# Kernel optimization log

Hardware: AMD Instinct MI355X
Metric: run time of the kernel (lower is better)

## Reference

```python
import jax, jax.numpy as jnp
import numpy as np

NEAR_ZERO = 1e-6


def hat(w):
    # [..., 3] -> [..., 3, 3] skew-symmetric
    x, y, z = w[..., 0], w[..., 1], w[..., 2]
    O = jnp.zeros_like(x)
    return jnp.stack([jnp.stack([O, -z, y], -1),
                      jnp.stack([z, O, -x], -1),
                      jnp.stack([-y, x, O], -1)], -2)


def matrix_exp6(V):
    # V: [..., 6] twist (w, v) -> [..., 4, 4] SE(3) exp, with near-zero branch as in the torch code
    w, v = V[..., :3], V[..., 3:]
    theta = jnp.linalg.norm(w, axis=-1, keepdims=True)  # [..., 1]
    near = theta < NEAR_ZERO
    safe = jnp.where(near, 1.0, theta)
    Wh = hat(w / safe)
    Wh2 = Wh @ Wh
    t = theta[..., None]  # [..., 1, 1]
    I3 = jnp.eye(3, dtype=V.dtype)
    R = I3 + jnp.sin(t) * Wh + (1.0 - jnp.cos(t)) * Wh2
    R = jnp.where(near[..., None], I3, R)
    G = t * I3 + (1.0 - jnp.cos(t)) * Wh + (t - jnp.sin(t)) * Wh2
    p = jnp.einsum('...ij,...j->...i', G, v / safe)
    p = jnp.where(near, v, p)
    top = jnp.concatenate([R, p[..., None]], -1)
    bot = jnp.broadcast_to(jnp.array([0.0, 0.0, 0.0, 1.0], V.dtype), top.shape[:-2] + (1, 4))
    return jnp.concatenate([top, bot], -2)


def trans_inv(T):
    R = T[..., :3, :3]
    p = T[..., :3, 3]
    Rt = jnp.swapaxes(R, -1, -2)
    pinv = -jnp.einsum('...ij,...j->...i', Rt, p)
    top = jnp.concatenate([Rt, pinv[..., None]], -1)
    bot = jnp.broadcast_to(jnp.array([0.0, 0.0, 0.0, 1.0], T.dtype), top.shape[:-2] + (1, 4))
    return jnp.concatenate([top, bot], -2)


def adjoint(T):
    R = T[..., :3, :3]
    p = T[..., :3, 3]
    Z = jnp.zeros_like(R)
    top = jnp.concatenate([R, Z], -1)
    bot = jnp.concatenate([hat(p) @ R, R], -1)
    return jnp.concatenate([top, bot], -2)


def ad(V):
    W = hat(V[..., :3])
    Vh = hat(V[..., 3:])
    Z = jnp.zeros_like(W)
    top = jnp.concatenate([W, Z], -1)
    bot = jnp.concatenate([Vh, W], -1)
    return jnp.concatenate([top, bot], -2)


def inverse_dynamics(q, dq, ddq, g, Ftip, Alist, Mlist, Glist):
    # q, dq, ddq: [B, JN]; g: [3]; Ftip: [B, 6]; Alist: [JN, 6]; Mlist: [JN+1, 4, 4]; Glist: [JN, 6, 6]
    B, JN = q.shape
    Minv = trans_inv(Mlist)  # [JN+1, 4, 4]
    v0 = jnp.zeros((B, 6), q.dtype)
    a0 = jnp.concatenate([jnp.zeros((B, 3), q.dtype), jnp.broadcast_to(-g, (B, 3))], -1)

    # forward recursion over joints (sequential -> lax.scan), vectorized over batch
    def fwd_step(carry, xs):
        v, a = carry
        A_i, Minv_i, q_i, dq_i, ddq_i = xs
        T = matrix_exp6(-A_i[None, :] * q_i[:, None]) @ Minv_i  # [B, 4, 4]
        Ad = adjoint(T)
        v_new = jnp.einsum('bij,bj->bi', Ad, v) + A_i * dq_i[:, None]
        a_new = (jnp.einsum('bij,bj->bi', Ad, a)
                 + jnp.einsum('bij,j->bi', ad(v_new), A_i) * dq_i[:, None]
                 + A_i * ddq_i[:, None])
        return (v_new, a_new), (T, v_new, a_new)

    _, (Ts, vs, as_) = jax.lax.scan(fwd_step, (v0, a0), (Alist, Minv[:-1], q.T, dq.T, ddq.T))
    T_last = jnp.broadcast_to(Minv[-1], (B, 4, 4))
    AdNext = adjoint(jnp.concatenate([Ts[1:], T_last[None]], 0))  # [JN, B, 6, 6]

    # backward force recursion
    def bwd_step(F, xs):
        AdN, G_i, A_i, v_i, a_i = xs
        F_new = (jnp.einsum('bji,bj->bi', AdN, F)
                 + jnp.einsum('ij,bj->bi', G_i, a_i)
                 - jnp.einsum('bji,jk,bk->bi', ad(v_i), G_i, v_i))
        return F_new, F_new @ A_i

    _, tau = jax.lax.scan(bwd_step, Ftip, (AdNext, Glist, Alist, vs, as_), reverse=True)
    return tau.T  # [B, JN]


def setup_inputs() -> dict:
    key = jax.random.key(0)
    k = jax.random.split(key, 8)
    B, JN = 131072, 9
    q = jax.random.normal(k[0], (B, JN), jnp.float32)
    dq = jax.random.normal(k[1], (B, JN), jnp.float32)
    ddq = jax.random.normal(k[2], (B, JN), jnp.float32)
    Ftip = jax.random.normal(k[3], (B, 6), jnp.float32)
    g = jnp.array([0.0, 0.0, -9.8], jnp.float32)
    # screw axes with unit rotational part (revolute joints)
    w = jax.random.normal(k[4], (JN, 3), jnp.float32)
    w = w / jnp.linalg.norm(w, axis=-1, keepdims=True)
    vlin = jax.random.normal(k[5], (JN, 3), jnp.float32)
    Alist = jnp.concatenate([w, vlin], -1)
    # valid SE(3) home transforms
    Mlist = matrix_exp6(0.5 * jax.random.normal(k[6], (JN + 1, 6), jnp.float32))
    # SPD spatial inertias
    S = 0.3 * jax.random.normal(k[7], (JN, 6, 6), jnp.float32)
    Glist = S @ jnp.swapaxes(S, -1, -2) + jnp.eye(6, dtype=jnp.float32)
    return {"q": q, "dq": dq, "ddq": ddq, "g": g, "Ftip": Ftip,
            "Alist": Alist, "Mlist": Mlist, "Glist": Glist}


def reference(q, dq, ddq, g, Ftip, Alist, Mlist, Glist):
    return inverse_dynamics(q, dq, ddq, g, Ftip, Alist, Mlist, Glist)
```

## Files before the change

### kernel.cpp

```cpp
#include <hip/hip_runtime.h>
#include <math.h>

#define JN 9
#define BLK 128
#define BLK_FB 128
#define CPJ 84
#define CST_FLOATS (JN * CPJ + 12)

__device__ __forceinline__ void mat3_vec(const float* R, const float* x, float* y) {
    y[0] = R[0]*x[0] + R[1]*x[1] + R[2]*x[2];
    y[1] = R[3]*x[0] + R[4]*x[1] + R[5]*x[2];
    y[2] = R[6]*x[0] + R[7]*x[1] + R[8]*x[2];
}
__device__ __forceinline__ void mat3T_vec(const float* R, const float* x, float* y) {
    y[0] = R[0]*x[0] + R[3]*x[1] + R[6]*x[2];
    y[1] = R[1]*x[0] + R[4]*x[1] + R[7]*x[2];
    y[2] = R[2]*x[0] + R[5]*x[1] + R[8]*x[2];
}
__device__ __forceinline__ void cross3(const float* a, const float* b, float* o) {
    o[0] = a[1]*b[2] - a[2]*b[1];
    o[1] = a[2]*b[0] - a[0]*b[2];
    o[2] = a[0]*b[1] - a[1]*b[0];
}
__device__ __forceinline__ void adj_apply(const float* R, const float* p,
                                          const float* x, float* y) {
    float t[3], cr[3], rv[3];
    mat3_vec(R, x, t);
    cross3(p, t, cr);
    mat3_vec(R, x + 3, rv);
    y[0] = t[0]; y[1] = t[1]; y[2] = t[2];
    y[3] = cr[0] + rv[0]; y[4] = cr[1] + rv[1]; y[5] = cr[2] + rv[2];
}
__device__ __forceinline__ void adjT_apply(const float* R, const float* p,
                                           const float* x, float* y) {
    float cr[3], t[3];
    cross3(p, x + 3, cr);
    t[0] = x[0] - cr[0]; t[1] = x[1] - cr[1]; t[2] = x[2] - cr[2];
    mat3T_vec(R, t, y);
    mat3T_vec(R, x + 3, y + 3);
}

__global__ void prep_kernel(const float* __restrict__ A, const float* __restrict__ M,
                            const float* __restrict__ G, float* __restrict__ cst) {
    const int j = threadIdx.x;
    if (j < JN) {
        const float* Aj = A + j * 6;
        const float* Mj = M + j * 16;
        const float ax = Aj[0], ay = Aj[1], az = Aj[2];
        const float vx = Aj[3], vy = Aj[4], vz = Aj[5];
        float M1[9];
        for (int t = 0; t < 3; ++t)
            for (int c = 0; c < 3; ++c) M1[t*3+c] = Mj[c*4+t];
        const float K[9] = {0.f,-az,ay, az,0.f,-ax, -ay,ax,0.f};
        float M2[9];
        for (int r = 0; r < 3; ++r)
            for (int c = 0; c < 3; ++c)
                M2[r*3+c] = K[r*3+0]*M1[0*3+c] + K[r*3+1]*M1[1*3+c] + K[r*3+2]*M1[2*3+c];
        float t3[3];
        for (int c = 0; c < 3; ++c) t3[c] = ax*M1[0*3+c] + ay*M1[1*3+c] + az*M1[2*3+c];
        float M3[9];
        const float Aw[3] = {ax, ay, az};
        for (int r = 0; r < 3; ++r)
            for (int c = 0; c < 3; ++c) M3[r*3+c] = Aw[r] * t3[c];
        float Q1[9], Q3[9];
        for (int e = 0; e < 9; ++e) { Q1[e] = M1[e] - M3[e]; Q3[e] = M3[e]; }
        const float Mp[3] = {Mj[3], Mj[7], Mj[11]};
        const float d = ax*vx + ay*vy + az*vz;
        const float C[3] = {ay*vz - az*vy, az*vx - ax*vz, ax*vy - ay*vx};
        float q2m[3], q1m[3], q3m[3];
        mat3_vec(M2, Mp, q2m);
        mat3_vec(Q1, Mp, q1m);
        mat3_vec(Q3, Mp, q3m);
        float* o = cst + j * CPJ;
        for (int e = 0; e < 9; ++e) { o[e] = Q1[e]; o[9+e] = M2[e]; o[18+e] = Q3[e]; }
        o[27] = (vx - d*ax) - q2m[0]; o[28] = (vy - d*ay) - q2m[1]; o[29] = (vz - d*az) - q2m[2];
        o[30] = -C[0] - q1m[0];       o[31] = -C[1] - q1m[1];       o[32] = -C[2] - q1m[2];
        o[33] = d*ax;                 o[34] = d*ay;                 o[35] = d*az;
        o[36] = C[0] - q3m[0];        o[37] = C[1] - q3m[1];        o[38] = C[2] - q3m[2];
        for (int k = 0; k < 6; ++k)  o[39 + k] = Aj[k];
        const float* Gj = G + j * 36;
        for (int k = 0; k < 36; ++k) o[45 + k] = Gj[k];
    } else if (j == JN) {
        const float* M9 = M + JN * 16;
        float* o = cst + JN * CPJ;
        for (int r = 0; r < 3; ++r)
            for (int c = 0; c < 3; ++c) o[r*3+c] = M9[c*4+r];
        o[9] = M9[3]; o[10] = M9[7]; o[11] = M9[11];
    }
}

__device__ __forceinline__ void joint_step(const float* __restrict__ Cj,
                                           float qj, float dqj, float ddqj,
                                           float* XR, float* Xp, float* bv,
                                           float* ba, float* U,
                                           float* Bv, float* sig_out)
{
    const float phi = -qj;
    float s, c;
    __sincosf(phi, &s, &c);

    float TR[9], Tp[3];
#pragma unroll
    for (int e = 0; e < 9; ++e) TR[e] = c * Cj[e] + s * Cj[9 + e] + Cj[18 + e];
#pragma unroll
    for (int k = 0; k < 3; ++k)
        Tp[k] = s * Cj[27 + k] + c * Cj[30 + k] + phi * Cj[33 + k] + Cj[36 + k];

    {
        float nR[9], np[3];
#pragma unroll
        for (int r = 0; r < 3; ++r)
#pragma unroll
            for (int cc = 0; cc < 3; ++cc)
                nR[r*3+cc] = TR[r*3+0]*XR[0*3+cc] + TR[r*3+1]*XR[1*3+cc] + TR[r*3+2]*XR[2*3+cc];
        mat3_vec(TR, Xp, np);
#pragma unroll
        for (int e = 0; e < 9; ++e) XR[e] = nR[e];
        Xp[0] = np[0] + Tp[0]; Xp[1] = np[1] + Tp[1]; Xp[2] = np[2] + Tp[2];
    }

    const float Aw[3] = {Cj[39], Cj[40], Cj[41]};
    const float Av[3] = {Cj[42], Cj[43], Cj[44]};
    {
        float ip[3], tw[3], tv[3], cr[3];
        mat3T_vec(XR, Xp, ip);
        ip[0] = -ip[0]; ip[1] = -ip[1]; ip[2] = -ip[2];
        mat3T_vec(XR, Aw, tw);
        mat3T_vec(XR, Av, tv);
        cross3(ip, tw, cr);
        Bv[0] = tw[0]; Bv[1] = tw[1]; Bv[2] = tw[2];
        Bv[3] = cr[0] + tv[0]; Bv[4] = cr[1] + tv[1]; Bv[5] = cr[2] + tv[2];
    }

    *sig_out = Bv[0]*U[0] + Bv[1]*U[1] + Bv[2]*U[2]
             + Bv[3]*U[3] + Bv[4]*U[4] + Bv[5]*U[5];

#pragma unroll
    for (int k = 0; k < 6; ++k) bv[k] += Bv[k] * dqj;
    {
        float t0[3], t1[3], t2[3];
        cross3(bv, Bv, t0);
        cross3(bv + 3, Bv, t1);
        cross3(bv, Bv + 3, t2);
        ba[0] += t0[0]*dqj + Bv[0]*ddqj;
        ba[1] += t0[1]*dqj + Bv[1]*ddqj;
        ba[2] += t0[2]*dqj + Bv[2]*ddqj;
        ba[3] += (t1[0]+t2[0])*dqj + Bv[3]*ddqj;
        ba[4] += (t1[1]+t2[1])*dqj + Bv[4]*ddqj;
        ba[5] += (t1[2]+t2[2])*dqj + Bv[5]*ddqj;
    }

    float vl[6], al[6];
    adj_apply(XR, Xp, bv, vl);
    adj_apply(XR, Xp, ba, al);
    float Gv[6], Ga[6];
#pragma unroll
    for (int r = 0; r < 6; ++r) {
        float sv = 0.f, sa = 0.f;
#pragma unroll
        for (int kk = 0; kk < 6; ++kk) {
            const float gmv = Cj[45 + r*6 + kk];
            sv += gmv * vl[kk];
            sa += gmv * al[kk];
        }
        Gv[r] = sv; Ga[r] = sa;
    }
    float W[6];
    {
        float cw[3], cv[3], cb[3];
        cross3(vl, Gv, cw);
        cross3(vl + 3, Gv + 3, cv);
        cross3(vl, Gv + 3, cb);
        W[0] = Ga[0]+cw[0]+cv[0]; W[1] = Ga[1]+cw[1]+cv[1]; W[2] = Ga[2]+cw[2]+cv[2];
        W[3] = Ga[3]+cb[0];       W[4] = Ga[4]+cb[1];       W[5] = Ga[5]+cb[2];
    }
    {
        float S[6];
        adjT_apply(XR, Xp, W, S);
#pragma unroll
        for (int k = 0; k < 6; ++k) U[k] += S[k];
    }
}

__device__ __forceinline__ void tail_E(const float* __restrict__ W9,
                                       const float* XR, const float* Xp,
                                       const float* Ft, const float* U, float* E)
{
    float R9[9], p9[3];
#pragma unroll
    for (int r = 0; r < 3; ++r)
#pragma unroll
        for (int cc = 0; cc < 3; ++cc)
            R9[r*3+cc] = W9[r*3+0]*XR[0*3+cc] + W9[r*3+1]*XR[1*3+cc] + W9[r*3+2]*XR[2*3+cc];
    const float t[3] = {Xp[0] - W9[9], Xp[1] - W9[10], Xp[2] - W9[11]};
    mat3_vec(W9, t, p9);
    float Z[6];
    adjT_apply(R9, p9, Ft, Z);
#pragma unroll
    for (int k = 0; k < 6; ++k) E[k] = U[k] + Z[k];
}

__global__ void __launch_bounds__(BLK)
id_main(const float* __restrict__ q, const float* __restrict__ dq,
        const float* __restrict__ ddq, const float* __restrict__ gvec,
        const float* __restrict__ Ftip, const float* __restrict__ cst,
        float* __restrict__ out, int B)
{
    __shared__ float sQ[JN][BLK + 1];
    __shared__ float sB[JN * 6][BLK];
    __shared__ float sSig[JN][BLK];

    const int tid = threadIdx.x;
    const int b = blockIdx.x * BLK + tid;
    const float g0 = gvec[0], g1 = gvec[1], g2 = gvec[2];

#pragma unroll
    for (int j = 0; j < JN; ++j) sQ[j][tid] = q[(size_t)b * JN + j];

    float XR[9] = {1.f,0.f,0.f, 0.f,1.f,0.f, 0.f,0.f,1.f};
    float Xp[3] = {0.f, 0.f, 0.f};
    float bv[6] = {0.f,0.f,0.f,0.f,0.f,0.f};
    float ba[6] = {0.f, 0.f, 0.f, -g0, -g1, -g2};
    float U[6]  = {0.f,0.f,0.f,0.f,0.f,0.f};

#pragma unroll 1
    for (int j = 0; j < JN; ++j) {
        const float dqj  = dq[(size_t)b * JN + j];
        const float ddqj = ddq[(size_t)b * JN + j];
        const float qj   = sQ[j][tid];
        const float* Cj = cst + j * CPJ;
        float Bv[6], sg;
        joint_step(Cj, qj, dqj, ddqj, XR, Xp, bv, ba, U, Bv, &sg);
#pragma unroll
        for (int k = 0; k < 6; ++k) sB[j*6 + k][tid] = Bv[k];
        sSig[j][tid] = sg;
    }

    const float* W9 = cst + JN * CPJ;
    float Ft[6];
    __builtin_memcpy(Ft, Ftip + (size_t)b * 6, 6 * sizeof(float));
    float E[6];
    tail_E(W9, XR, Xp, Ft, U, E);

#pragma unroll
    for (int i = 0; i < JN; ++i) {
        float d = -sSig[i][tid];
#pragma unroll
        for (int k = 0; k < 6; ++k) d += sB[i*6 + k][tid] * E[k];
        sQ[i][tid] = d;
    }
    __syncthreads();
    const size_t base = (size_t)blockIdx.x * BLK * JN;
#pragma unroll
    for (int k = 0; k < JN; ++k) {
        const int g = tid + k * BLK;
        out[base + g] = sQ[g % JN][g / JN];
    }
}

__global__ void __launch_bounds__(BLK_FB)
id_kernel_fb(const float* __restrict__ q, const float* __restrict__ dq,
             const float* __restrict__ ddq, const float* __restrict__ gvec,
             const float* __restrict__ Ftip, const float* __restrict__ Alist,
             const float* __restrict__ Mlist, const float* __restrict__ Glist,
             float* __restrict__ out, int B)
{
    __shared__ float sB[JN * 6][BLK_FB];
    __shared__ float sSig[JN][BLK_FB];
    const int tid = threadIdx.x;
    const int b = blockIdx.x * BLK_FB + tid;
    if (b >= B) return;
    float XR[9] = {1.f,0.f,0.f, 0.f,1.f,0.f, 0.f,0.f,1.f};
    float Xp[3] = {0.f, 0.f, 0.f};
    float bv[6] = {0.f,0.f,0.f,0.f,0.f,0.f};
    float ba[6] = {0.f, 0.f, 0.f, -gvec[0], -gvec[1], -gvec[2]};
    float U[6]  = {0.f,0.f,0.f,0.f,0.f,0.f};
#pragma unroll 1
    for (int j = 0; j < JN; ++j) {
        const float* Am = Alist + j * 6;
        const float* Gm = Glist + j * 36;
        const float* Mj = Mlist + j * 16;
        float Aj[6];
#pragma unroll
        for (int k = 0; k < 6; ++k) Aj[k] = Am[k];
        const float qj = q[b*JN+j], dqj = dq[b*JN+j], ddqj = ddq[b*JN+j];
        const float w0 = -Aj[0]*qj, w1 = -Aj[1]*qj, w2 = -Aj[2]*qj;
        const float l0 = -Aj[3]*qj, l1 = -Aj[4]*qj, l2 = -Aj[5]*qj;
        const float th = sqrtf(w0*w0 + w1*w1 + w2*w2);
        const bool near = th < 1e-6f;
        const float safe = near ? 1.f : th;
        const float inv = __builtin_amdgcn_rcpf(safe);
        const float x = w0*inv, y = w1*inv, z = w2*inv;
        const float st = __sinf(th), ct = __cosf(th);
        const float s2 = 1.f - ct;
        const float a00 = -(z*z+y*y), a11 = -(z*z+x*x), a22 = -(y*y+x*x);
        const float a01 = x*y, a02 = x*z, a12 = y*z;
        float R[9];
        R[0]=1.f+s2*a00;   R[1]=-st*z+s2*a01; R[2]= st*y+s2*a02;
        R[3]= st*z+s2*a01; R[4]=1.f+s2*a11;   R[5]=-st*x+s2*a12;
        R[6]=-st*y+s2*a02; R[7]= st*x+s2*a12; R[8]=1.f+s2*a22;
        if (near) { R[0]=1;R[1]=0;R[2]=0;R[3]=0;R[4]=1;R[5]=0;R[6]=0;R[7]=0;R[8]=1; }
        const float g3 = th - st;
        const float u0 = l0*inv, u1 = l1*inv, u2 = l2*inv;
        float p0 = th*u0 + s2*(-z*u1+y*u2) + g3*(a00*u0+a01*u1+a02*u2);
        float p1 = th*u1 + s2*( z*u0-x*u2) + g3*(a01*u0+a11*u1+a12*u2);
        float p2 = th*u2 + s2*(-y*u0+x*u1) + g3*(a02*u0+a12*u1+a22*u2);
        if (near) { p0=l0; p1=l1; p2=l2; }
        float TR[9], Tp[3];
#pragma unroll
        for (int r = 0; r < 3; ++r)
#pragma unroll
            for (int cc = 0; cc < 3; ++cc)
                TR[r*3+cc] = R[r*3+0]*Mj[cc*4+0] + R[r*3+1]*Mj[cc*4+1] + R[r*3+2]*Mj[cc*4+2];
        const float mp0 = Mj[3], mp1 = Mj[7], mp2 = Mj[11];
        Tp[0] = p0 - (TR[0]*mp0 + TR[1]*mp1 + TR[2]*mp2);
        Tp[1] = p1 - (TR[3]*mp0 + TR[4]*mp1 + TR[5]*mp2);
        Tp[2] = p2 - (TR[6]*mp0 + TR[7]*mp1 + TR[8]*mp2);
        {
            float nR[9], np[3];
#pragma unroll
            for (int r = 0; r < 3; ++r)
#pragma unroll
                for (int cc = 0; cc < 3; ++cc)
                    nR[r*3+cc] = TR[r*3+0]*XR[0*3+cc] + TR[r*3+1]*XR[1*3+cc] + TR[r*3+2]*XR[2*3+cc];
            mat3_vec(TR, Xp, np);
#pragma unroll
            for (int e = 0; e < 9; ++e) XR[e] = nR[e];
            Xp[0] = np[0]+Tp[0]; Xp[1] = np[1]+Tp[1]; Xp[2] = np[2]+Tp[2];
        }
        float Bv[6];
        {
            float ip[3], tw[3], tvv[3], cr[3];
            mat3T_vec(XR, Xp, ip);
            ip[0]=-ip[0]; ip[1]=-ip[1]; ip[2]=-ip[2];
            mat3T_vec(XR, Aj, tw);
            mat3T_vec(XR, Aj+3, tvv);
            cross3(ip, tw, cr);
            Bv[0]=tw[0]; Bv[1]=tw[1]; Bv[2]=tw[2];
            Bv[3]=cr[0]+tvv[0]; Bv[4]=cr[1]+tvv[1]; Bv[5]=cr[2]+tvv[2];
        }
        float sg = Bv[0]*U[0]+Bv[1]*U[1]+Bv[2]*U[2]+Bv[3]*U[3]+Bv[4]*U[4]+Bv[5]*U[5];
#pragma unroll
        for (int k = 0; k < 6; ++k) bv[k] += Bv[k]*dqj;
        {
            float t0[3], t1[3], t2[3];
            cross3(bv, Bv, t0); cross3(bv+3, Bv, t1); cross3(bv, Bv+3, t2);
            ba[0] += t0[0]*dqj + Bv[0]*ddqj;
            ba[1] += t0[1]*dqj + Bv[1]*ddqj;
            ba[2] += t0[2]*dqj + Bv[2]*ddqj;
            ba[3] += (t1[0]+t2[0])*dqj + Bv[3]*ddqj;
            ba[4] += (t1[1]+t2[1])*dqj + Bv[4]*ddqj;
            ba[5] += (t1[2]+t2[2])*dqj + Bv[5]*ddqj;
        }
        float vl[6], al[6];
        adj_apply(XR, Xp, bv, vl);
        adj_apply(XR, Xp, ba, al);
        float Gv[6], Ga[6];
#pragma unroll
        for (int r = 0; r < 6; ++r) {
            float sv = 0.f, sa = 0.f;
#pragma unroll
            for (int kk = 0; kk < 6; ++kk) { sv += Gm[r*6+kk]*vl[kk]; sa += Gm[r*6+kk]*al[kk]; }
            Gv[r] = sv; Ga[r] = sa;
        }
        float W[6];
        {
            float cw[3], cv[3], cb[3];
            cross3(vl, Gv, cw); cross3(vl+3, Gv+3, cv); cross3(vl, Gv+3, cb);
            W[0]=Ga[0]+cw[0]+cv[0]; W[1]=Ga[1]+cw[1]+cv[1]; W[2]=Ga[2]+cw[2]+cv[2];
            W[3]=Ga[3]+cb[0];       W[4]=Ga[4]+cb[1];       W[5]=Ga[5]+cb[2];
        }
        {
            float S[6];
            adjT_apply(XR, Xp, W, S);
#pragma unroll
            for (int k = 0; k < 6; ++k) U[k] += S[k];
        }
#pragma unroll
        for (int k = 0; k < 6; ++k) sB[j*6+k][tid] = Bv[k];
        sSig[j][tid] = sg;
    }
    float E[6];
    {
        const float* M9 = Mlist + JN * 16;
        float R9[9], p9[3];
#pragma unroll
        for (int r = 0; r < 3; ++r)
#pragma unroll
            for (int cc = 0; cc < 3; ++cc)
                R9[r*3+cc] = M9[0*4+r]*XR[0*3+cc] + M9[1*4+r]*XR[1*3+cc] + M9[2*4+r]*XR[2*3+cc];
        float t[3] = {Xp[0]-M9[3], Xp[1]-M9[7], Xp[2]-M9[11]};
        p9[0] = M9[0]*t[0] + M9[4]*t[1] + M9[8]*t[2];
        p9[1] = M9[1]*t[0] + M9[5]*t[1] + M9[9]*t[2];
        p9[2] = M9[2]*t[0] + M9[6]*t[1] + M9[10]*t[2];
        float Ftl[6];
#pragma unroll
        for (int k = 0; k < 6; ++k) Ftl[k] = Ftip[b*6+k];
        float Z[6];
        adjT_apply(R9, p9, Ftl, Z);
#pragma unroll
        for (int k = 0; k < 6; ++k) E[k] = U[k] + Z[k];
    }
#pragma unroll
    for (int i = 0; i < JN; ++i) {
        float d = -sSig[i][tid];
#pragma unroll
        for (int k = 0; k < 6; ++k) d += sB[i*6+k][tid] * E[k];
        out[b*JN+i] = d;
    }
}

extern "C" void kernel_launch(void* const* d_in, const int* in_sizes, int n_in,
                              void* d_out, int out_size, void* d_ws, size_t ws_size,
                              hipStream_t stream) {
    const float* q     = (const float*)d_in[0];
    const float* dq    = (const float*)d_in[1];
    const float* ddq   = (const float*)d_in[2];
    const float* g     = (const float*)d_in[3];
    const float* Ftip  = (const float*)d_in[4];
    const float* Alist = (const float*)d_in[5];
    const float* Mlist = (const float*)d_in[6];
    const float* Glist = (const float*)d_in[7];
    float* out = (float*)d_out;
    const int B = in_sizes[0] / JN;

    if (ws_size >= CST_FLOATS * sizeof(float) && (B % BLK) == 0) {
        float* cst = (float*)d_ws;
        hipLaunchKernelGGL(prep_kernel, dim3(1), dim3(16), 0, stream,
                           Alist, Mlist, Glist, cst);
        const int grid = B / BLK;
        hipLaunchKernelGGL(id_main, dim3(grid), dim3(BLK), 0, stream,
                           q, dq, ddq, g, Ftip, cst, out, B);
    } else {
        const int grid = (B + BLK_FB - 1) / BLK_FB;
        hipLaunchKernelGGL(id_kernel_fb, dim3(grid), dim3(BLK_FB), 0, stream,
                           q, dq, ddq, g, Ftip, Alist, Mlist, Glist, out, B);
    }
}
```

Measured before the change: 30.01 us.

## Drop prep kernel and compute per-joint transforms inline in main kernel

Removes the separate single-thread prep kernel that precomputed per-joint constant coefficients, and instead computes the SE(3) exponential and home-transform product inside the main kernel directly from Alist/Mlist/Glist. It also stages q through shared memory with coalesced loads, reuses sQ for the sigma values in place of a separate buffer, and writes the output directly per thread rather than transposing it through shared memory. This saves one kernel launch and the dependency between the two kernels, at the cost of more per-thread arithmetic (sqrt, rcp, sin/cos, 3x3 products) and uncoalesced output stores.

```diff
diff --git a/kernel.cpp b/kernel.cpp
--- a/kernel.cpp
+++ b/kernel.cpp
@@ -3,9 +3,6 @@
 
 #define JN 9
 #define BLK 128
-#define BLK_FB 128
-#define CPJ 84
-#define CST_FLOATS (JN * CPJ + 12)
 
 __device__ __forceinline__ void mat3_vec(const float* R, const float* x, float* y) {
     y[0] = R[0]*x[0] + R[1]*x[1] + R[2]*x[2];
@@ -40,183 +37,33 @@
     mat3T_vec(R, x + 3, y + 3);
 }
 
-__global__ void prep_kernel(const float* __restrict__ A, const float* __restrict__ M,
-                            const float* __restrict__ G, float* __restrict__ cst) {
-    const int j = threadIdx.x;
-    if (j < JN) {
-        const float* Aj = A + j * 6;
-        const float* Mj = M + j * 16;
-        const float ax = Aj[0], ay = Aj[1], az = Aj[2];
-        const float vx = Aj[3], vy = Aj[4], vz = Aj[5];
-        float M1[9];
-        for (int t = 0; t < 3; ++t)
-            for (int c = 0; c < 3; ++c) M1[t*3+c] = Mj[c*4+t];
-        const float K[9] = {0.f,-az,ay, az,0.f,-ax, -ay,ax,0.f};
-        float M2[9];
-        for (int r = 0; r < 3; ++r)
-            for (int c = 0; c < 3; ++c)
-                M2[r*3+c] = K[r*3+0]*M1[0*3+c] + K[r*3+1]*M1[1*3+c] + K[r*3+2]*M1[2*3+c];
-        float t3[3];
-        for (int c = 0; c < 3; ++c) t3[c] = ax*M1[0*3+c] + ay*M1[1*3+c] + az*M1[2*3+c];
-        float M3[9];
-        const float Aw[3] = {ax, ay, az};
-        for (int r = 0; r < 3; ++r)
-            for (int c = 0; c < 3; ++c) M3[r*3+c] = Aw[r] * t3[c];
-        float Q1[9], Q3[9];
-        for (int e = 0; e < 9; ++e) { Q1[e] = M1[e] - M3[e]; Q3[e] = M3[e]; }
-        const float Mp[3] = {Mj[3], Mj[7], Mj[11]};
-        const float d = ax*vx + ay*vy + az*vz;
-        const float C[3] = {ay*vz - az*vy, az*vx - ax*vz, ax*vy - ay*vx};
-        float q2m[3], q1m[3], q3m[3];
-        mat3_vec(M2, Mp, q2m);
-        mat3_vec(Q1, Mp, q1m);
-        mat3_vec(Q3, Mp, q3m);
-        float* o = cst + j * CPJ;
-        for (int e = 0; e < 9; ++e) { o[e] = Q1[e]; o[9+e] = M2[e]; o[18+e] = Q3[e]; }
-        o[27] = (vx - d*ax) - q2m[0]; o[28] = (vy - d*ay) - q2m[1]; o[29] = (vz - d*az) - q2m[2];
-        o[30] = -C[0] - q1m[0];       o[31] = -C[1] - q1m[1];       o[32] = -C[2] - q1m[2];
-        o[33] = d*ax;                 o[34] = d*ay;                 o[35] = d*az;
-        o[36] = C[0] - q3m[0];        o[37] = C[1] - q3m[1];        o[38] = C[2] - q3m[2];
-        for (int k = 0; k < 6; ++k)  o[39 + k] = Aj[k];
-        const float* Gj = G + j * 36;
-        for (int k = 0; k < 36; ++k) o[45 + k] = Gj[k];
-    } else if (j == JN) {
-        const float* M9 = M + JN * 16;
-        float* o = cst + JN * CPJ;
-        for (int r = 0; r < 3; ++r)
-            for (int c = 0; c < 3; ++c) o[r*3+c] = M9[c*4+r];
-        o[9] = M9[3]; o[10] = M9[7]; o[11] = M9[11];
-    }
-}
-
-__device__ __forceinline__ void joint_step(const float* __restrict__ Cj,
-                                           float qj, float dqj, float ddqj,
-                                           float* XR, float* Xp, float* bv,
-                                           float* ba, float* U,
-                                           float* Bv, float* sig_out)
-{
-    const float phi = -qj;
-    float s, c;
-    __sincosf(phi, &s, &c);
-
-    float TR[9], Tp[3];
-#pragma unroll
-    for (int e = 0; e < 9; ++e) TR[e] = c * Cj[e] + s * Cj[9 + e] + Cj[18 + e];
-#pragma unroll
-    for (int k = 0; k < 3; ++k)
-        Tp[k] = s * Cj[27 + k] + c * Cj[30 + k] + phi * Cj[33 + k] + Cj[36 + k];
-
-    {
-        float nR[9], np[3];
-#pragma unroll
-        for (int r = 0; r < 3; ++r)
-#pragma unroll
-            for (int cc = 0; cc < 3; ++cc)
-                nR[r*3+cc] = TR[r*3+0]*XR[0*3+cc] + TR[r*3+1]*XR[1*3+cc] + TR[r*3+2]*XR[2*3+cc];
-        mat3_vec(TR, Xp, np);
-#pragma unroll
-        for (int e = 0; e < 9; ++e) XR[e] = nR[e];
-        Xp[0] = np[0] + Tp[0]; Xp[1] = np[1] + Tp[1]; Xp[2] = np[2] + Tp[2];
-    }
-
-    const float Aw[3] = {Cj[39], Cj[40], Cj[41]};
-    const float Av[3] = {Cj[42], Cj[43], Cj[44]};
-    {
-        float ip[3], tw[3], tv[3], cr[3];
-        mat3T_vec(XR, Xp, ip);
-        ip[0] = -ip[0]; ip[1] = -ip[1]; ip[2] = -ip[2];
-        mat3T_vec(XR, Aw, tw);
-        mat3T_vec(XR, Av, tv);
-        cross3(ip, tw, cr);
-        Bv[0] = tw[0]; Bv[1] = tw[1]; Bv[2] = tw[2];
-        Bv[3] = cr[0] + tv[0]; Bv[4] = cr[1] + tv[1]; Bv[5] = cr[2] + tv[2];
-    }
-
-    *sig_out = Bv[0]*U[0] + Bv[1]*U[1] + Bv[2]*U[2]
-             + Bv[3]*U[3] + Bv[4]*U[4] + Bv[5]*U[5];
-
-#pragma unroll
-    for (int k = 0; k < 6; ++k) bv[k] += Bv[k] * dqj;
-    {
-        float t0[3], t1[3], t2[3];
-        cross3(bv, Bv, t0);
-        cross3(bv + 3, Bv, t1);
-        cross3(bv, Bv + 3, t2);
-        ba[0] += t0[0]*dqj + Bv[0]*ddqj;
-        ba[1] += t0[1]*dqj + Bv[1]*ddqj;
-        ba[2] += t0[2]*dqj + Bv[2]*ddqj;
-        ba[3] += (t1[0]+t2[0])*dqj + Bv[3]*ddqj;
-        ba[4] += (t1[1]+t2[1])*dqj + Bv[4]*ddqj;
-        ba[5] += (t1[2]+t2[2])*dqj + Bv[5]*ddqj;
-    }
-
-    float vl[6], al[6];
-    adj_apply(XR, Xp, bv, vl);
-    adj_apply(XR, Xp, ba, al);
-    float Gv[6], Ga[6];
-#pragma unroll
-    for (int r = 0; r < 6; ++r) {
-        float sv = 0.f, sa = 0.f;
-#pragma unroll
-        for (int kk = 0; kk < 6; ++kk) {
-            const float gmv = Cj[45 + r*6 + kk];
-            sv += gmv * vl[kk];
-            sa += gmv * al[kk];
-        }
-        Gv[r] = sv; Ga[r] = sa;
-    }
-    float W[6];
-    {
-        float cw[3], cv[3], cb[3];
-        cross3(vl, Gv, cw);
-        cross3(vl + 3, Gv + 3, cv);
-        cross3(vl, Gv + 3, cb);
-        W[0] = Ga[0]+cw[0]+cv[0]; W[1] = Ga[1]+cw[1]+cv[1]; W[2] = Ga[2]+cw[2]+cv[2];
-        W[3] = Ga[3]+cb[0];       W[4] = Ga[4]+cb[1];       W[5] = Ga[5]+cb[2];
-    }
-    {
-        float S[6];
-        adjT_apply(XR, Xp, W, S);
-#pragma unroll
-        for (int k = 0; k < 6; ++k) U[k] += S[k];
-    }
-}
-
-__device__ __forceinline__ void tail_E(const float* __restrict__ W9,
-                                       const float* XR, const float* Xp,
-                                       const float* Ft, const float* U, float* E)
-{
-    float R9[9], p9[3];
-#pragma unroll
-    for (int r = 0; r < 3; ++r)
-#pragma unroll
-        for (int cc = 0; cc < 3; ++cc)
-            R9[r*3+cc] = W9[r*3+0]*XR[0*3+cc] + W9[r*3+1]*XR[1*3+cc] + W9[r*3+2]*XR[2*3+cc];
-    const float t[3] = {Xp[0] - W9[9], Xp[1] - W9[10], Xp[2] - W9[11]};
-    mat3_vec(W9, t, p9);
-    float Z[6];
-    adjT_apply(R9, p9, Ft, Z);
-#pragma unroll
-    for (int k = 0; k < 6; ++k) E[k] = U[k] + Z[k];
-}
-
 __global__ void __launch_bounds__(BLK)
 id_main(const float* __restrict__ q, const float* __restrict__ dq,
         const float* __restrict__ ddq, const float* __restrict__ gvec,
-        const float* __restrict__ Ftip, const float* __restrict__ cst,
+        const float* __restrict__ Ftip, const float* __restrict__ Alist,
+        const float* __restrict__ Mlist, const float* __restrict__ Glist,
         float* __restrict__ out, int B)
 {
     __shared__ float sQ[JN][BLK + 1];
     __shared__ float sB[JN * 6][BLK];
-    __shared__ float sSig[JN][BLK];
 
     const int tid = threadIdx.x;
     const int b = blockIdx.x * BLK + tid;
+
+    {
+        const float* qBlk = q + (size_t)blockIdx.x * BLK * JN;
+#pragma unroll
+        for (int k = 0; k < JN; ++k) {
+            const int m = k * BLK + tid;
+            sQ[m % JN][m / JN] = qBlk[m];
+        }
+    }
+    __syncthreads();
+
+    float Ft[6];
+    __builtin_memcpy(Ft, Ftip + (size_t)b * 6, 6 * sizeof(float));
+
     const float g0 = gvec[0], g1 = gvec[1], g2 = gvec[2];
-
-#pragma unroll
-    for (int j = 0; j < JN; ++j) sQ[j][tid] = q[(size_t)b * JN + j];
-
     float XR[9] = {1.f,0.f,0.f, 0.f,1.f,0.f, 0.f,0.f,1.f};
     float Xp[3] = {0.f, 0.f, 0.f};
     float bv[6] = {0.f,0.f,0.f,0.f,0.f,0.f};
@@ -225,50 +72,162 @@
 
 #pragma unroll 1
     for (int j = 0; j < JN; ++j) {
+        const float* Am = Alist + j * 6;
+        const float* Gm = Glist + j * 36;
+        const float* Mj = Mlist + j * 16;
+        float Aj[6];
+#pragma unroll
+        for (int k = 0; k < 6; ++k) Aj[k] = Am[k];
+
+        const float qj   = sQ[j][tid];
         const float dqj  = dq[(size_t)b * JN + j];
         const float ddqj = ddq[(size_t)b * JN + j];
-        const float qj   = sQ[j][tid];
-        const float* Cj = cst + j * CPJ;
-        float Bv[6], sg;
-        joint_step(Cj, qj, dqj, ddqj, XR, Xp, bv, ba, U, Bv, &sg);
-#pragma unroll
-        for (int k = 0; k < 6; ++k) sB[j*6 + k][tid] = Bv[k];
-        sSig[j][tid] = sg;
-    }
-
-    const float* W9 = cst + JN * CPJ;
-    float Ft[6];
-    __builtin_memcpy(Ft, Ftip + (size_t)b * 6, 6 * sizeof(float));
+
+        const float w0 = -Aj[0]*qj, w1 = -Aj[1]*qj, w2 = -Aj[2]*qj;
+        const float l0 = -Aj[3]*qj, l1 = -Aj[4]*qj, l2 = -Aj[5]*qj;
+        const float th = sqrtf(w0*w0 + w1*w1 + w2*w2);
+        const bool near = th < 1e-6f;
+        const float safe = near ? 1.f : th;
+        const float inv = __builtin_amdgcn_rcpf(safe);
+        const float x = w0*inv, y = w1*inv, z = w2*inv;
+        const float st = __sinf(th), ct = __cosf(th);
+        const float s2 = 1.f - ct;
+        const float a00 = -(z*z+y*y), a11 = -(z*z+x*x), a22 = -(y*y+x*x);
+        const float a01 = x*y, a02 = x*z, a12 = y*z;
+        float R[9];
+        R[0]=1.f+s2*a00;   R[1]=-st*z+s2*a01; R[2]= st*y+s2*a02;
+        R[3]= st*z+s2*a01; R[4]=1.f+s2*a11;   R[5]=-st*x+s2*a12;
+        R[6]=-st*y+s2*a02; R[7]= st*x+s2*a12; R[8]=1.f+s2*a22;
+        if (near) { R[0]=1;R[1]=0;R[2]=0;R[3]=0;R[4]=1;R[5]=0;R[6]=0;R[7]=0;R[8]=1; }
+        const float g3 = th - st;
+        const float u0 = l0*inv, u1 = l1*inv, u2 = l2*inv;
+        float p0 = th*u0 + s2*(-z*u1+y*u2) + g3*(a00*u0+a01*u1+a02*u2);
+        float p1 = th*u1 + s2*( z*u0-x*u2) + g3*(a01*u0+a11*u1+a12*u2);
+        float p2 = th*u2 + s2*(-y*u0+x*u1) + g3*(a02*u0+a12*u1+a22*u2);
+        if (near) { p0=l0; p1=l1; p2=l2; }
+
+        float TR[9], Tp[3];
+        {
+#pragma unroll
+            for (int r = 0; r < 3; ++r)
+#pragma unroll
+                for (int cc = 0; cc < 3; ++cc)
+                    TR[r*3+cc] = R[r*3+0]*Mj[cc*4+0] + R[r*3+1]*Mj[cc*4+1] + R[r*3+2]*Mj[cc*4+2];
+            const float mp0 = Mj[3], mp1 = Mj[7], mp2 = Mj[11];
+            Tp[0] = p0 - (TR[0]*mp0 + TR[1]*mp1 + TR[2]*mp2);
+            Tp[1] = p1 - (TR[3]*mp0 + TR[4]*mp1 + TR[5]*mp2);
+            Tp[2] = p2 - (TR[6]*mp0 + TR[7]*mp1 + TR[8]*mp2);
+        }
+
+        {
+            float nR[9], np[3];
+#pragma unroll
+            for (int r = 0; r < 3; ++r)
+#pragma unroll
+                for (int cc = 0; cc < 3; ++cc)
+                    nR[r*3+cc] = TR[r*3+0]*XR[0*3+cc] + TR[r*3+1]*XR[1*3+cc] + TR[r*3+2]*XR[2*3+cc];
+            mat3_vec(TR, Xp, np);
+#pragma unroll
+            for (int e = 0; e < 9; ++e) XR[e] = nR[e];
+            Xp[0] = np[0]+Tp[0]; Xp[1] = np[1]+Tp[1]; Xp[2] = np[2]+Tp[2];
+        }
+
+        float Bv[6];
+        {
+            float ip[3], tw[3], tv[3], cr[3];
+            mat3T_vec(XR, Xp, ip);
+            ip[0]=-ip[0]; ip[1]=-ip[1]; ip[2]=-ip[2];
+            mat3T_vec(XR, Aj, tw);
+            mat3T_vec(XR, Aj+3, tv);
+            cross3(ip, tw, cr);
+            Bv[0]=tw[0]; Bv[1]=tw[1]; Bv[2]=tw[2];
+            Bv[3]=cr[0]+tv[0]; Bv[4]=cr[1]+tv[1]; Bv[5]=cr[2]+tv[2];
+        }
+
+        const float sg = Bv[0]*U[0]+Bv[1]*U[1]+Bv[2]*U[2]
+                       + Bv[3]*U[3]+Bv[4]*U[4]+Bv[5]*U[5];
+
+#pragma unroll
+        for (int k = 0; k < 6; ++k) bv[k] += Bv[k]*dqj;
+        {
+            float t0[3], t1[3], t2[3];
+            cross3(bv, Bv, t0); cross3(bv+3, Bv, t1); cross3(bv, Bv+3, t2);
+            ba[0] += t0[0]*dqj + Bv[0]*ddqj;
+            ba[1] += t0[1]*dqj + Bv[1]*ddqj;
+            ba[2] += t0[2]*dqj + Bv[2]*ddqj;
+            ba[3] += (t1[0]+t2[0])*dqj + Bv[3]*ddqj;
+            ba[4] += (t1[1]+t2[1])*dqj + Bv[4]*ddqj;
+            ba[5] += (t1[2]+t2[2])*dqj + Bv[5]*ddqj;
+        }
+
+        float vl[6], al[6];
+        adj_apply(XR, Xp, bv, vl);
+        adj_apply(XR, Xp, ba, al);
+        float Gv[6], Ga[6];
+#pragma unroll
+        for (int r = 0; r < 6; ++r) {
+            float sv = 0.f, sa = 0.f;
+#pragma unroll
+            for (int kk = 0; kk < 6; ++kk) { sv += Gm[r*6+kk]*vl[kk]; sa += Gm[r*6+kk]*al[kk]; }
+            Gv[r] = sv; Ga[r] = sa;
+        }
+        float W[6];
+        {
+            float cw[3], cv[3], cb[3];
+            cross3(vl, Gv, cw); cross3(vl+3, Gv+3, cv); cross3(vl, Gv+3, cb);
+            W[0]=Ga[0]+cw[0]+cv[0]; W[1]=Ga[1]+cw[1]+cv[1]; W[2]=Ga[2]+cw[2]+cv[2];
+            W[3]=Ga[3]+cb[0];       W[4]=Ga[4]+cb[1];       W[5]=Ga[5]+cb[2];
+        }
+        {
+            float S[6];
+            adjT_apply(XR, Xp, W, S);
+#pragma unroll
+            for (int k = 0; k < 6; ++k) U[k] += S[k];
+        }
+
+#pragma unroll
+        for (int k = 0; k < 6; ++k) sB[j*6+k][tid] = Bv[k];
+        sQ[j][tid] = sg;
+    }
+
     float E[6];
-    tail_E(W9, XR, Xp, Ft, U, E);
-
+    {
+        const float* M9 = Mlist + JN * 16;
+        float R9[9], p9[3];
+#pragma unroll
+        for (int r = 0; r < 3; ++r)
+#pragma unroll
+            for (int cc = 0; cc < 3; ++cc)
+                R9[r*3+cc] = M9[0*4+r]*XR[0*3+cc] + M9[1*4+r]*XR[1*3+cc] + M9[2*4+r]*XR[2*3+cc];
+        float t[3] = {Xp[0]-M9[3], Xp[1]-M9[7], Xp[2]-M9[11]};
+        p9[0] = M9[0]*t[0] + M9[4]*t[1] + M9[8]*t[2];
+        p9[1] = M9[1]*t[0] + M9[5]*t[1] + M9[9]*t[2];
+        p9[2] = M9[2]*t[0] + M9[6]*t[1] + M9[10]*t[2];
+        float Z[6];
+        adjT_apply(R9, p9, Ft, Z);
+#pragma unroll
+        for (int k = 0; k < 6; ++k) E[k] = U[k] + Z[k];
+    }
 #pragma unroll
     for (int i = 0; i < JN; ++i) {
-        float d = -sSig[i][tid];
-#pragma unroll
-        for (int k = 0; k < 6; ++k) d += sB[i*6 + k][tid] * E[k];
-        sQ[i][tid] = d;
-    }
-    __syncthreads();
-    const size_t base = (size_t)blockIdx.x * BLK * JN;
-#pragma unroll
-    for (int k = 0; k < JN; ++k) {
-        const int g = tid + k * BLK;
-        out[base + g] = sQ[g % JN][g / JN];
-    }
-}
-
-__global__ void __launch_bounds__(BLK_FB)
+        float d = -sQ[i][tid];
+#pragma unroll
+        for (int k = 0; k < 6; ++k) d += sB[i*6+k][tid] * E[k];
+        out[(size_t)b*JN + i] = d;
+    }
+}
+
+__global__ void __launch_bounds__(BLK)
 id_kernel_fb(const float* __restrict__ q, const float* __restrict__ dq,
              const float* __restrict__ ddq, const float* __restrict__ gvec,
              const float* __restrict__ Ftip, const float* __restrict__ Alist,
              const float* __restrict__ Mlist, const float* __restrict__ Glist,
              float* __restrict__ out, int B)
 {
-    __shared__ float sB[JN * 6][BLK_FB];
-    __shared__ float sSig[JN][BLK_FB];
+    __shared__ float sB[JN * 6][BLK];
+    __shared__ float sSig[JN][BLK];
     const int tid = threadIdx.x;
-    const int b = blockIdx.x * BLK_FB + tid;
+    const int b = blockIdx.x * BLK + tid;
     if (b >= B) return;
     float XR[9] = {1.f,0.f,0.f, 0.f,1.f,0.f, 0.f,0.f,1.f};
     float Xp[3] = {0.f, 0.f, 0.f};
@@ -424,16 +383,13 @@
     float* out = (float*)d_out;
     const int B = in_sizes[0] / JN;
 
-    if (ws_size >= CST_FLOATS * sizeof(float) && (B % BLK) == 0) {
-        float* cst = (float*)d_ws;
-        hipLaunchKernelGGL(prep_kernel, dim3(1), dim3(16), 0, stream,
-                           Alist, Mlist, Glist, cst);
+    if ((B % BLK) == 0) {
         const int grid = B / BLK;
         hipLaunchKernelGGL(id_main, dim3(grid), dim3(BLK), 0, stream,
-                           q, dq, ddq, g, Ftip, cst, out, B);
+                           q, dq, ddq, g, Ftip, Alist, Mlist, Glist, out, B);
     } else {
-        const int grid = (B + BLK_FB - 1) / BLK_FB;
-        hipLaunchKernelGGL(id_kernel_fb, dim3(grid), dim3(BLK_FB), 0, stream,
+        const int grid = (B + BLK - 1) / BLK;
+        hipLaunchKernelGGL(id_kernel_fb, dim3(grid), dim3(BLK), 0, stream,
                            q, dq, ddq, g, Ftip, Alist, Mlist, Glist, out, B);
     }
 }
```

Measured after the change: 27.09 us. 9.7% less time.
